# Optimization experiments

Hardware: AMD Instinct MI355X
Metric: run time of the kernel (lower is better)

Reference implementation:

```python
import jax, jax.numpy as jnp
import numpy as np

B, S, HID = 2, 2048, 1024
HEADS, DHEAD = 16, 64
INNER = HEADS * DHEAD


def setup_inputs() -> dict:
    key = jax.random.key(0)
    ks = jax.random.split(key, 12)
    s = 0.02
    return {
        "query": jax.random.normal(ks[0], (B, S, HID), jnp.float32),
        "key": jax.random.normal(ks[1], (B, S, HID), jnp.float32),
        "value": jax.random.normal(ks[2], (B, S, HID), jnp.float32),
        "mask": jnp.zeros((B, 1, S, S), jnp.float32),
        "position_bias": jax.random.normal(ks[3], (1, HEADS, S, S), jnp.float32),
        "Wq": jax.random.normal(ks[4], (HID, INNER), jnp.float32) * s,
        "bq": jnp.zeros((INNER,), jnp.float32),
        "Wk": jax.random.normal(ks[5], (HID, INNER), jnp.float32) * s,
        "bk": jnp.zeros((INNER,), jnp.float32),
        "Wv": jax.random.normal(ks[6], (HID, INNER), jnp.float32) * s,
        "bv": jnp.zeros((INNER,), jnp.float32),
        "Wo": jax.random.normal(ks[7], (INNER, HID), jnp.float32) * s,
        "bo": jnp.zeros((HID,), jnp.float32),
    }


def reference(query, key, value, mask, position_bias,
              Wq, bq, Wk, bk, Wv, bv, Wo, bo):
    # project and split heads: [B,S,HID] -> [B,HEADS,S,DHEAD]
    def shape(x, W, b):
        return (x @ W + b).reshape(B, S, HEADS, DHEAD).transpose(0, 2, 1, 3)

    q = shape(query, Wq, bq)
    k = shape(key, Wk, bk)
    v = shape(value, Wv, bv)

    scores = jnp.einsum("bhqd,bhkd->bhqk", q, k)
    scores = scores + position_bias          # bias added BEFORE scaling (as in source)
    scores = scores / jnp.sqrt(jnp.float32(DHEAD))
    scores = scores + mask                   # additive mask
    probs = jax.nn.softmax(scores, axis=-1)  # dropout p=0.0 -> identity

    out = jnp.einsum("bhqk,bhkd->bhqd", probs, v)
    out = out.transpose(0, 2, 1, 3).reshape(B, S, INNER)
    return out @ Wo + bo
```

## Files before the change

### kernel.cpp

```cpp
#include <hip/hip_runtime.h>
#include <cstdint>
#include <cstddef>

#define B_SZ      2
#define S_LEN     2048
#define HID_DIM   1024
#define N_HEAD    16
#define D_HEAD    64
#define INNER_DIM 1024

#define C1 0.18033688011112042f
#define C2 1.44269504088896340736f

typedef __attribute__((ext_vector_type(8))) short bf16x8;
typedef __attribute__((ext_vector_type(4))) float f32x4;

__device__ __forceinline__ unsigned short f2bf(float f) {
  unsigned int u = __float_as_uint(f);
  u += 0x7fffu + ((u >> 16) & 1u);
  return (unsigned short)(u >> 16);
}
__device__ __forceinline__ float bf2f(unsigned short u) {
  return __uint_as_float(((unsigned int)u) << 16);
}

__device__ __forceinline__ void gload_lds16(const void* g, void* l) {
  __builtin_amdgcn_global_load_lds((const __attribute__((address_space(1))) void*)g,
                                   (__attribute__((address_space(3))) void*)l,
                                   16, 0, 0);
}

__global__ void cast3_kernel(const float* __restrict__ i0, const float* __restrict__ i1,
                             const float* __restrict__ i2,
                             unsigned short* __restrict__ o0, unsigned short* __restrict__ o1,
                             unsigned short* __restrict__ o2, int n4) {
  int z = blockIdx.y;
  const float* in = (z == 0) ? i0 : (z == 1) ? i1 : i2;
  unsigned short* out = (z == 0) ? o0 : (z == 1) ? o1 : o2;
  int i = blockIdx.x * blockDim.x + threadIdx.x;
  if (i < n4) {
    float4 v = ((const float4*)in)[i];
    ushort4 o;
    o.x = f2bf(v.x); o.y = f2bf(v.y); o.z = f2bf(v.z); o.w = f2bf(v.w);
    ((ushort4*)out)[i] = o;
  }
}

__global__ void transpose_cast_kernel(const float* __restrict__ in,
                                      unsigned short* __restrict__ out,
                                      int rows, int cols) {
  __shared__ float tile[32][33];
  int bx = blockIdx.x * 32;
  int by = blockIdx.y * 32;
  int tx = threadIdx.x & 31;
  int ty = threadIdx.x >> 5;
#pragma unroll
  for (int i = 0; i < 32; i += 8)
    tile[ty + i][tx] = in[(size_t)(by + ty + i) * cols + bx + tx];
  __syncthreads();
#pragma unroll
  for (int i = 0; i < 32; i += 8)
    out[(size_t)(bx + ty + i) * rows + by + tx] = f2bf(tile[tx][ty + i]);
}


__global__ __launch_bounds__(256, 2)
void qkv_gemm_kernel(const unsigned short* __restrict__ Aq,
                     const unsigned short* __restrict__ Ak,
                     const unsigned short* __restrict__ Av,
                     const unsigned short* __restrict__ Wq,
                     const unsigned short* __restrict__ Wk,
                     const unsigned short* __restrict__ Wv,
                     const float* __restrict__ bq,
                     const float* __restrict__ bk,
                     const float* __restrict__ bv,
                     unsigned short* __restrict__ Oq,
                     unsigned short* __restrict__ Ok,
                     unsigned short* __restrict__ Ov) {
  constexpr int K = 1024;
  __shared__ unsigned short Asm[128 * 64];
  __shared__ unsigned short Bsm[64 * 64];

  const int z = blockIdx.z;
  const unsigned short* A  = (z == 0) ? Aq : (z == 1) ? Ak : Av;
  const unsigned short* Bt = (z == 0) ? Wq : (z == 1) ? Wk : Wv;
  const float* bias        = (z == 0) ? bq : (z == 1) ? bk : bv;
  const float scale        = (z == 0) ? C1 : 1.0f;

  const int tid = threadIdx.x;
  const int lane = tid & 63;
  const int w = tid >> 6;
  const int wm = w & 1;
  const int wn = w >> 1;
  const int c = lane & 15;
  const int g = lane >> 4;
  const int m0 = blockIdx.x * 128;
  const int n0 = blockIdx.y * 64;

  f32x4 acc[4][2];
  f32x4 zero = {0.f, 0.f, 0.f, 0.f};
#pragma unroll
  for (int mt = 0; mt < 4; ++mt)
#pragma unroll
    for (int nt = 0; nt < 2; ++nt) acc[mt][nt] = zero;

  for (int kk = 0; kk < K / 64; ++kk) {
    __syncthreads();
    const int k0 = kk * 64;
#pragma unroll
    for (int it = 0; it < 4; ++it) {
      int slot = it * 256 + tid;
      int r = slot >> 3, sp = slot & 7, seg = sp ^ (r & 7);
      gload_lds16(A + (size_t)(m0 + r) * K + k0 + seg * 8,
                  (char*)Asm + (it * 256 + w * 64) * 16);
    }
#pragma unroll
    for (int it = 0; it < 2; ++it) {
      int slot = it * 256 + tid;
      int r = slot >> 3, sp = slot & 7, seg = sp ^ (r & 7);
      gload_lds16(Bt + (size_t)(n0 + r) * K + k0 + seg * 8,
                  (char*)Bsm + (it * 256 + w * 64) * 16);
    }
    __syncthreads();

#pragma unroll
    for (int ks = 0; ks < 2; ++ks) {
      bf16x8 aF[4];
#pragma unroll
      for (int mt = 0; mt < 4; ++mt) {
        int r = wm * 64 + mt * 16 + c;
        int seg = (ks * 4 + g) ^ (r & 7);
        aF[mt] = *(const bf16x8*)((const char*)Asm + r * 128 + seg * 16);
      }
#pragma unroll
      for (int nt = 0; nt < 2; ++nt) {
        int r = wn * 32 + nt * 16 + c;
        int seg = (ks * 4 + g) ^ (r & 7);
        bf16x8 bF = *(const bf16x8*)((const char*)Bsm + r * 128 + seg * 16);
#pragma unroll
        for (int mt = 0; mt < 4; ++mt)
          acc[mt][nt] = __builtin_amdgcn_mfma_f32_16x16x32_bf16(aF[mt], bF, acc[mt][nt], 0, 0, 0);
      }
    }
  }

#pragma unroll
  for (int nt = 0; nt < 2; ++nt) {
    int n_g = n0 + wn * 32 + nt * 16 + c;
    float bvv = bias[n_g];
#pragma unroll
    for (int mt = 0; mt < 4; ++mt) {
      int m_base = m0 + wm * 64 + mt * 16 + g * 4;
      if (z == 2) {
        int b = m_base >> 11;
        int s = m_base & 2047;
        int hh = n_g >> 6;
        int d = n_g & 63;
        ushort4 pk;
        pk.x = f2bf(acc[mt][nt][0] + bvv);
        pk.y = f2bf(acc[mt][nt][1] + bvv);
        pk.z = f2bf(acc[mt][nt][2] + bvv);
        pk.w = f2bf(acc[mt][nt][3] + bvv);
        *(ushort4*)(Ov + ((size_t)((b * N_HEAD + hh) * D_HEAD + d)) * S_LEN + s) = pk;
      } else {
        unsigned short* o = (z == 0) ? Oq : Ok;
#pragma unroll
        for (int r = 0; r < 4; ++r)
          o[(size_t)(m_base + r) * INNER_DIM + n_g] = f2bf((acc[mt][nt][r] + bvv) * scale);
      }
    }
  }
}

__global__ __launch_bounds__(256, 2)
void out_gemm_kernel(const unsigned short* __restrict__ A,
                     const unsigned short* __restrict__ Bt,
                     const float* __restrict__ bias,
                     float* __restrict__ out) {
  constexpr int K = 1024;
  __shared__ unsigned short Asm[128 * 64];
  __shared__ unsigned short Bsm[64 * 64];

  const int tid = threadIdx.x;
  const int lane = tid & 63;
  const int w = tid >> 6;
  const int wm = w & 1;
  const int wn = w >> 1;
  const int c = lane & 15;
  const int g = lane >> 4;
  const int m0 = blockIdx.x * 128;
  const int n0 = blockIdx.y * 64;

  f32x4 acc[4][2];
  f32x4 zero = {0.f, 0.f, 0.f, 0.f};
#pragma unroll
  for (int mt = 0; mt < 4; ++mt)
#pragma unroll
    for (int nt = 0; nt < 2; ++nt) acc[mt][nt] = zero;

  for (int kk = 0; kk < K / 64; ++kk) {
    __syncthreads();
    const int k0 = kk * 64;
#pragma unroll
    for (int it = 0; it < 4; ++it) {
      int slot = it * 256 + tid;
      int r = slot >> 3, sp = slot & 7, seg = sp ^ (r & 7);
      gload_lds16(A + (size_t)(m0 + r) * K + k0 + seg * 8,
                  (char*)Asm + (it * 256 + w * 64) * 16);
    }
#pragma unroll
    for (int it = 0; it < 2; ++it) {
      int slot = it * 256 + tid;
      int r = slot >> 3, sp = slot & 7, seg = sp ^ (r & 7);
      gload_lds16(Bt + (size_t)(n0 + r) * K + k0 + seg * 8,
                  (char*)Bsm + (it * 256 + w * 64) * 16);
    }
    __syncthreads();

#pragma unroll
    for (int ks = 0; ks < 2; ++ks) {
      bf16x8 aF[4];
#pragma unroll
      for (int mt = 0; mt < 4; ++mt) {
        int r = wm * 64 + mt * 16 + c;
        int seg = (ks * 4 + g) ^ (r & 7);
        aF[mt] = *(const bf16x8*)((const char*)Asm + r * 128 + seg * 16);
      }
#pragma unroll
      for (int nt = 0; nt < 2; ++nt) {
        int r = wn * 32 + nt * 16 + c;
        int seg = (ks * 4 + g) ^ (r & 7);
        bf16x8 bF = *(const bf16x8*)((const char*)Bsm + r * 128 + seg * 16);
#pragma unroll
        for (int mt = 0; mt < 4; ++mt)
          acc[mt][nt] = __builtin_amdgcn_mfma_f32_16x16x32_bf16(aF[mt], bF, acc[mt][nt], 0, 0, 0);
      }
    }
  }

#pragma unroll
  for (int nt = 0; nt < 2; ++nt) {
    int n_g = n0 + wn * 32 + nt * 16 + c;
    float bvv = bias[n_g];
#pragma unroll
    for (int mt = 0; mt < 4; ++mt) {
      int m_base = m0 + wm * 64 + mt * 16 + g * 4;
#pragma unroll
      for (int r = 0; r < 4; ++r)
        out[(size_t)(m_base + r) * HID_DIM + n_g] = acc[mt][nt][r] + bvv;
    }
  }
}

__global__ __launch_bounds__(512, 4)
void attn_kernel(const unsigned short* __restrict__ Qp,
                 const unsigned short* __restrict__ Kp,
                 const unsigned short* __restrict__ Vp,
                 const float* __restrict__ bias,
                 const float* __restrict__ mask,
                 unsigned short* __restrict__ Osm) {
  __shared__ unsigned short Ksm[128 * 64];
  __shared__ unsigned short Vsm[64 * 128];
  __shared__ unsigned short Psm[128 * 128];

  const int tid = threadIdx.x;
  const int lane = tid & 63;
  const int w = tid >> 6;
  const int c = lane & 15;
  const int g = lane >> 4;
  const int q0 = blockIdx.x * 128;
  const int h = blockIdx.y;
  const int b = blockIdx.z;

  char* Pw = (char*)Psm + w * 4096;

  bf16x8 qF[2];
  {
    size_t row = (size_t)(b * S_LEN + q0 + w * 16 + c);
#pragma unroll
    for (int ks = 0; ks < 2; ++ks)
      qF[ks] = *(const bf16x8*)(Qp + row * INNER_DIM + h * D_HEAD + ks * 32 + g * 8);
  }

  const int lrow = lane >> 5;
  const int lcol = lane & 31;
  const float* bias_base = bias + ((size_t)h * S_LEN + q0 + w * 16 + lrow) * S_LEN + lcol * 4;
  const float* mask_base = mask + ((size_t)b * S_LEN + q0 + w * 16 + lrow) * S_LEN + lcol * 4;

  float m_run[4], l_run[4];
  f32x4 oacc[4];
  f32x4 zero = {0.f, 0.f, 0.f, 0.f};
#pragma unroll
  for (int r = 0; r < 4; ++r) { m_run[r] = -1e30f; l_run[r] = 0.f; }
#pragma unroll
  for (int dt = 0; dt < 4; ++dt) oacc[dt] = zero;

  for (int j = 0; j < S_LEN / 128; ++j) {
    __syncthreads();
#pragma unroll
    for (int it = 0; it < 2; ++it) {
      int slot = it * 512 + tid;
      int r = slot >> 3, sp = slot & 7, seg = sp ^ (r & 7);
      gload_lds16(Kp + (size_t)(b * S_LEN + j * 128 + r) * INNER_DIM + h * D_HEAD + seg * 8,
                  (char*)Ksm + (it * 512 + w * 64) * 16);
    }
#pragma unroll
    for (int it = 0; it < 2; ++it) {
      int slot = it * 512 + tid;
      int r = slot >> 4, sp = slot & 15, seg = sp ^ (r & 15);
      gload_lds16(Vp + ((size_t)((b * N_HEAD + h) * D_HEAD + r)) * S_LEN + j * 128 + seg * 8,
                  (char*)Vsm + (it * 512 + w * 64) * 16);
    }

#pragma unroll
    for (int half = 0; half < 2; ++half) {
      float4 bl[4], ml[4];
#pragma unroll
      for (int p = 0; p < 4; ++p) {
        int pp = half * 4 + p;
        bl[p] = *(const float4*)(bias_base + (size_t)(pp * 2) * S_LEN + j * 128);
        ml[p] = *(const float4*)(mask_base + (size_t)(pp * 2) * S_LEN + j * 128);
      }
#pragma unroll
      for (int p = 0; p < 4; ++p) {
        int pp = half * 4 + p;
        ushort4 fo;
        fo.x = f2bf(bl[p].x * C1 + ml[p].x * C2);
        fo.y = f2bf(bl[p].y * C1 + ml[p].y * C2);
        fo.z = f2bf(bl[p].z * C1 + ml[p].z * C2);
        fo.w = f2bf(bl[p].w * C1 + ml[p].w * C2);
        *(ushort4*)(Pw + (pp * 2 + lrow) * 256 + lcol * 8) = fo;
      }
    }
    __syncthreads();

    f32x4 sAcc[8];
#pragma unroll
    for (int nt = 0; nt < 8; ++nt) sAcc[nt] = zero;
#pragma unroll
    for (int ks = 0; ks < 2; ++ks)
#pragma unroll
      for (int nt = 0; nt < 8; ++nt) {
        int r = nt * 16 + c;
        int seg = (ks * 4 + g) ^ (r & 7);
        bf16x8 kF = *(const bf16x8*)((const char*)Ksm + r * 128 + seg * 16);
        sAcc[nt] = __builtin_amdgcn_mfma_f32_16x16x32_bf16(qF[ks], kF, sAcc[nt], 0, 0, 0);
      }

#pragma unroll
    for (int nt = 0; nt < 8; ++nt)
#pragma unroll
      for (int r = 0; r < 4; ++r) {
        int row_l = g * 4 + r;
        int kv_l = nt * 16 + c;
        sAcc[nt][r] += bf2f(*(const unsigned short*)(Pw + row_l * 256 + kv_l * 2));
      }

#pragma unroll
    for (int r = 0; r < 4; ++r) {
      float mx = sAcc[0][r];
#pragma unroll
      for (int nt = 1; nt < 8; ++nt) mx = fmaxf(mx, sAcc[nt][r]);
      mx = fmaxf(mx, __shfl_xor(mx, 1));
      mx = fmaxf(mx, __shfl_xor(mx, 2));
      mx = fmaxf(mx, __shfl_xor(mx, 4));
      mx = fmaxf(mx, __shfl_xor(mx, 8));
      float mnew = fmaxf(m_run[r], mx);
      float alpha = __builtin_amdgcn_exp2f(m_run[r] - mnew);
      m_run[r] = mnew;
      float ssum = 0.f;
#pragma unroll
      for (int nt = 0; nt < 8; ++nt) {
        float pv = __builtin_amdgcn_exp2f(sAcc[nt][r] - mnew);
        sAcc[nt][r] = pv;
        ssum += pv;
      }
      ssum += __shfl_xor(ssum, 1);
      ssum += __shfl_xor(ssum, 2);
      ssum += __shfl_xor(ssum, 4);
      ssum += __shfl_xor(ssum, 8);
      l_run[r] = l_run[r] * alpha + ssum;
#pragma unroll
      for (int dt = 0; dt < 4; ++dt) oacc[dt][r] *= alpha;
    }

#pragma unroll
    for (int nt = 0; nt < 8; ++nt)
#pragma unroll
      for (int r = 0; r < 4; ++r) {
        int row_l = g * 4 + r;
        int kv = nt * 16 + c;
        int seg = (kv >> 3) ^ row_l;
        *(unsigned short*)(Pw + row_l * 256 + seg * 16 + (kv & 7) * 2) = f2bf(sAcc[nt][r]);
      }

#pragma unroll
    for (int ks = 0; ks < 4; ++ks) {
      int segP = (ks * 4 + g) ^ c;
      bf16x8 aP = *(const bf16x8*)(Pw + c * 256 + segP * 16);
#pragma unroll
      for (int dt = 0; dt < 4; ++dt) {
        int dr = dt * 16 + c;
        int segV = (ks * 4 + g) ^ (dr & 15);
        bf16x8 vF = *(const bf16x8*)((const char*)Vsm + dr * 256 + segV * 16);
        oacc[dt] = __builtin_amdgcn_mfma_f32_16x16x32_bf16(aP, vF, oacc[dt], 0, 0, 0);
      }
    }
  }

#pragma unroll
  for (int r = 0; r < 4; ++r) {
    float inv = 1.f / l_run[r];
    int qg = q0 + w * 16 + g * 4 + r;
#pragma unroll
    for (int dt = 0; dt < 4; ++dt)
      Osm[(size_t)(b * S_LEN + qg) * INNER_DIM + h * D_HEAD + dt * 16 + c] =
          f2bf(oacc[dt][r] * inv);
  }
}

extern "C" void kernel_launch(void* const* d_in, const int* in_sizes, int n_in,
                              void* d_out, int out_size, void* d_ws, size_t ws_size,
                              hipStream_t stream) {
  const float* query = (const float*)d_in[0];
  const float* key   = (const float*)d_in[1];
  const float* value = (const float*)d_in[2];
  const float* mask  = (const float*)d_in[3];
  const float* bias  = (const float*)d_in[4];
  const float* Wq = (const float*)d_in[5];
  const float* bq = (const float*)d_in[6];
  const float* Wk = (const float*)d_in[7];
  const float* bk = (const float*)d_in[8];
  const float* Wv = (const float*)d_in[9];
  const float* bv = (const float*)d_in[10];
  const float* Wo = (const float*)d_in[11];
  const float* bo = (const float*)d_in[12];

  const size_t NTOK   = (size_t)B_SZ * S_LEN;
  const size_t SZ_ACT = NTOK * INNER_DIM;
  const size_t SZ_W   = (size_t)HID_DIM * INNER_DIM;

  unsigned short* ws  = (unsigned short*)d_ws;
  unsigned short* qb  = ws;
  unsigned short* kb  = qb + SZ_ACT;
  unsigned short* vb  = kb + SZ_ACT;
  unsigned short* Wqt = vb + SZ_ACT;
  unsigned short* Wkt = Wqt + SZ_W;
  unsigned short* Wvt = Wkt + SZ_W;
  unsigned short* Wot = Wvt + SZ_W;
  unsigned short* Qp  = Wot + SZ_W;
  unsigned short* Kp  = Qp + SZ_ACT;
  unsigned short* Vp  = Kp + SZ_ACT;
  unsigned short* Ob  = Vp + SZ_ACT;

  int n4 = (int)(SZ_ACT / 4);
  int cblk = (n4 + 255) / 256;
  dim3 cgrid(cblk, 3);
  cast3_kernel<<<cgrid, 256, 0, stream>>>(query, key, value, qb, kb, vb, n4);

  dim3 tgrid(INNER_DIM / 32, HID_DIM / 32);
  transpose_cast_kernel<<<tgrid, 256, 0, stream>>>(Wq, Wqt, HID_DIM, INNER_DIM);
  transpose_cast_kernel<<<tgrid, 256, 0, stream>>>(Wk, Wkt, HID_DIM, INNER_DIM);
  transpose_cast_kernel<<<tgrid, 256, 0, stream>>>(Wv, Wvt, HID_DIM, INNER_DIM);
  transpose_cast_kernel<<<tgrid, 256, 0, stream>>>(Wo, Wot, INNER_DIM, HID_DIM);

  dim3 ggrid(NTOK / 128, INNER_DIM / 64, 3);
  qkv_gemm_kernel<<<ggrid, 256, 0, stream>>>(qb, kb, vb, Wqt, Wkt, Wvt,
                                             bq, bk, bv, Qp, Kp, Vp);

  dim3 agrid(S_LEN / 128, N_HEAD, B_SZ);
  attn_kernel<<<agrid, 512, 0, stream>>>(Qp, Kp, Vp, bias, mask, Ob);

  dim3 ogrid(NTOK / 128, HID_DIM / 64);
  out_gemm_kernel<<<ogrid, 256, 0, stream>>>(Ob, Wot, bo, (float*)d_out);
}
```

Before: 647.7 us.

## Double-buffer K/V tiles in LDS and prefetch next bias tile into registers

The attention kernel now keeps two LDS buffers each for K and V. While computing on the current tile it issues the async global-to-LDS loads for the next tile, which lets it drop the second barrier per iteration. It also loads the next iteration's position-bias values into registers during the QK^T MFMAs, to hide global latency. In exchange LDS use per block grows by 32KB and register pressure rises, so launch bounds are relaxed to 2 blocks per CU and occupancy may fall.

```diff
diff --git a/kernel.cpp b/kernel.cpp
--- a/kernel.cpp
+++ b/kernel.cpp
@@ -252,15 +252,17 @@
   }
 }
 
-__global__ __launch_bounds__(512, 4)
+__global__ __launch_bounds__(512, 2)
 void attn_kernel(const unsigned short* __restrict__ Qp,
                  const unsigned short* __restrict__ Kp,
                  const unsigned short* __restrict__ Vp,
                  const float* __restrict__ bias,
                  const float* __restrict__ mask,
                  unsigned short* __restrict__ Osm) {
-  __shared__ unsigned short Ksm[128 * 64];
-  __shared__ unsigned short Vsm[64 * 128];
+  __shared__ unsigned short Ksm0[128 * 64];
+  __shared__ unsigned short Ksm1[128 * 64];
+  __shared__ unsigned short Vsm0[64 * 128];
+  __shared__ unsigned short Vsm1[64 * 128];
   __shared__ unsigned short Psm[128 * 128];
 
   const int tid = threadIdx.x;
@@ -287,6 +289,40 @@
   const float* bias_base = bias + ((size_t)h * S_LEN + q0 + w * 16 + lrow) * S_LEN + lcol * 4;
   const float* mask_base = mask + ((size_t)b * S_LEN + q0 + w * 16 + lrow) * S_LEN + lcol * 4;
 
+  const unsigned short* kSrc0;
+  const unsigned short* kSrc1;
+  const unsigned short* vSrc0;
+  const unsigned short* vSrc1;
+  {
+    int slot = tid;
+    int r = slot >> 3, sp = slot & 7, seg = sp ^ (r & 7);
+    kSrc0 = Kp + (size_t)(b * S_LEN + r) * INNER_DIM + h * D_HEAD + seg * 8;
+    slot = 512 + tid;
+    r = slot >> 3; sp = slot & 7; seg = sp ^ (r & 7);
+    kSrc1 = Kp + (size_t)(b * S_LEN + r) * INNER_DIM + h * D_HEAD + seg * 8;
+
+    slot = tid;
+    int rv = slot >> 4, spv = slot & 15, sgv = spv ^ (rv & 15);
+    vSrc0 = Vp + ((size_t)((b * N_HEAD + h) * D_HEAD + rv)) * S_LEN + sgv * 8;
+    slot = 512 + tid;
+    rv = slot >> 4; spv = slot & 15; sgv = spv ^ (rv & 15);
+    vSrc1 = Vp + ((size_t)((b * N_HEAD + h) * D_HEAD + rv)) * S_LEN + sgv * 8;
+  }
+
+  auto STAGE = [&](int jt, unsigned short* Kd, unsigned short* Vd) {
+    gload_lds16(kSrc0 + (size_t)jt * (128 * INNER_DIM), (char*)Kd + w * 1024);
+    gload_lds16(kSrc1 + (size_t)jt * (128 * INNER_DIM), (char*)Kd + 8192 + w * 1024);
+    gload_lds16(vSrc0 + jt * 128, (char*)Vd + w * 1024);
+    gload_lds16(vSrc1 + jt * 128, (char*)Vd + 8192 + w * 1024);
+  };
+
+  float4 bpre[8];
+  auto BIAS_PRE = [&](int jt) {
+#pragma unroll
+    for (int p = 0; p < 8; ++p)
+      bpre[p] = *(const float4*)(bias_base + (size_t)(p * 2) * S_LEN + jt * 128);
+  };
+
   float m_run[4], l_run[4];
   f32x4 oacc[4];
   f32x4 zero = {0.f, 0.f, 0.f, 0.f};
@@ -295,44 +331,38 @@
 #pragma unroll
   for (int dt = 0; dt < 4; ++dt) oacc[dt] = zero;
 
+  STAGE(0, Ksm0, Vsm0);
+  BIAS_PRE(0);
+
   for (int j = 0; j < S_LEN / 128; ++j) {
     __syncthreads();
-#pragma unroll
-    for (int it = 0; it < 2; ++it) {
-      int slot = it * 512 + tid;
-      int r = slot >> 3, sp = slot & 7, seg = sp ^ (r & 7);
-      gload_lds16(Kp + (size_t)(b * S_LEN + j * 128 + r) * INNER_DIM + h * D_HEAD + seg * 8,
-                  (char*)Ksm + (it * 512 + w * 64) * 16);
-    }
-#pragma unroll
-    for (int it = 0; it < 2; ++it) {
-      int slot = it * 512 + tid;
-      int r = slot >> 4, sp = slot & 15, seg = sp ^ (r & 15);
-      gload_lds16(Vp + ((size_t)((b * N_HEAD + h) * D_HEAD + r)) * S_LEN + j * 128 + seg * 8,
-                  (char*)Vsm + (it * 512 + w * 64) * 16);
-    }
+    const int pu = j & 1;
+    const unsigned short* Kc = pu ? Ksm1 : Ksm0;
+    const unsigned short* Vc = pu ? Vsm1 : Vsm0;
+    unsigned short* Kn = pu ? Ksm0 : Ksm1;
+    unsigned short* Vn = pu ? Vsm0 : Vsm1;
+    const int jn = (j + 1 < S_LEN / 128) ? j + 1 : j;
+
+    STAGE(jn, Kn, Vn);
 
 #pragma unroll
     for (int half = 0; half < 2; ++half) {
-      float4 bl[4], ml[4];
+      float4 ml[4];
+#pragma unroll
+      for (int p = 0; p < 4; ++p)
+        ml[p] = *(const float4*)(mask_base + (size_t)((half * 4 + p) * 2) * S_LEN + j * 128);
 #pragma unroll
       for (int p = 0; p < 4; ++p) {
         int pp = half * 4 + p;
-        bl[p] = *(const float4*)(bias_base + (size_t)(pp * 2) * S_LEN + j * 128);
-        ml[p] = *(const float4*)(mask_base + (size_t)(pp * 2) * S_LEN + j * 128);
-      }
-#pragma unroll
-      for (int p = 0; p < 4; ++p) {
-        int pp = half * 4 + p;
+        float4 bl = bpre[pp];
         ushort4 fo;
-        fo.x = f2bf(bl[p].x * C1 + ml[p].x * C2);
-        fo.y = f2bf(bl[p].y * C1 + ml[p].y * C2);
-        fo.z = f2bf(bl[p].z * C1 + ml[p].z * C2);
-        fo.w = f2bf(bl[p].w * C1 + ml[p].w * C2);
+        fo.x = f2bf(bl.x * C1 + ml[p].x * C2);
+        fo.y = f2bf(bl.y * C1 + ml[p].y * C2);
+        fo.z = f2bf(bl.z * C1 + ml[p].z * C2);
+        fo.w = f2bf(bl.w * C1 + ml[p].w * C2);
         *(ushort4*)(Pw + (pp * 2 + lrow) * 256 + lcol * 8) = fo;
       }
     }
-    __syncthreads();
 
     f32x4 sAcc[8];
 #pragma unroll
@@ -343,9 +373,11 @@
       for (int nt = 0; nt < 8; ++nt) {
         int r = nt * 16 + c;
         int seg = (ks * 4 + g) ^ (r & 7);
-        bf16x8 kF = *(const bf16x8*)((const char*)Ksm + r * 128 + seg * 16);
+        bf16x8 kF = *(const bf16x8*)((const char*)Kc + r * 128 + seg * 16);
         sAcc[nt] = __builtin_amdgcn_mfma_f32_16x16x32_bf16(qF[ks], kF, sAcc[nt], 0, 0, 0);
       }
+
+    BIAS_PRE(jn);
 
 #pragma unroll
     for (int nt = 0; nt < 8; ++nt)
@@ -402,7 +434,7 @@
       for (int dt = 0; dt < 4; ++dt) {
         int dr = dt * 16 + c;
         int segV = (ks * 4 + g) ^ (dr & 15);
-        bf16x8 vF = *(const bf16x8*)((const char*)Vsm + dr * 256 + segV * 16);
+        bf16x8 vF = *(const bf16x8*)((const char*)Vc + dr * 256 + segV * 16);
         oacc[dt] = __builtin_amdgcn_mfma_f32_16x16x32_bf16(aP, vF, oacc[dt], 0, 0, 0);
       }
     }
```

After: 604.6 us. 1.07x faster.
